# Kernel tuning notes

Hardware: AMD Instinct MI355X
Metric: run time of the kernel (lower is better)

Reference implementation:

```python
import jax, jax.numpy as jnp
import numpy as np

B, LH, LU, H = 32, 1024, 128, 256
NEG = -1e30


def setup_inputs() -> dict:
    key = jax.random.key(0)
    k1, k2, k3, k4, k5, k6 = jax.random.split(key, 6)
    h = jax.random.normal(k1, (B, LH, H), jnp.float32)
    u = jax.random.normal(k2, (B, LU, H), jnp.float32)
    # valid-prefix padding masks (at least half the sequence valid)
    h_len = jax.random.randint(k3, (B,), LH // 2, LH + 1)
    u_len = jax.random.randint(k4, (B,), LU // 2, LU + 1)
    h_mask = jnp.arange(LH)[None, :] < h_len[:, None]
    u_mask = jnp.arange(LU)[None, :] < u_len[:, None]
    # sim_proj: Linear(3H, 1) -> weight flattened to [3H], scalar bias
    w = jax.random.normal(k5, (3 * H,), jnp.float32) / np.sqrt(3 * H)
    b = jax.random.normal(k6, (), jnp.float32)
    return {"h": h, "u": u, "h_mask": h_mask, "u_mask": u_mask, "w": w, "b": b}


def reference(h, u, h_mask, u_mask, w, b):
    d = h.shape[-1]
    w_h, w_u, w_hu = w[:d], w[d:2 * d], w[2 * d:]
    # S[b,i,j] = [h_i; u_j; h_i*u_j] @ w + b  (decomposed, no [B,Lh,Lu,3H] blow-up)
    S = ((h @ w_h)[:, :, None]
         + (u @ w_u)[:, None, :]
         + jnp.einsum('bih,bjh->bij', h * w_hu, u)
         + b)  # [B, Lh, Lu]
    neg = jnp.asarray(NEG, S.dtype)
    # context-to-query attention: softmax over u (dim 2), masked by u_mask
    a_t = jax.nn.softmax(jnp.where(u_mask[:, None, :], S, neg), axis=2)  # [B,Lh,Lu]
    U_tilde = jnp.einsum('bij,bjh->bih', a_t, u)  # [B,Lh,H]
    # query-to-context attention: softmax over h (dim 1), masked by h_mask
    b_t = jax.nn.softmax(jnp.where(h_mask[:, :, None], S, neg), axis=1)  # [B,Lh,Lu]
    b2 = jnp.einsum('biu,bju->bij', b_t, a_t)  # [B,Lh,Lh] = b_t @ a_t^T
    H_tilde = jnp.einsum('bij,bjh->bih', b2, h)  # [B,Lh,H]
    return jnp.concatenate([h, U_tilde, h * U_tilde, h * H_tilde], axis=-1)
```

## Files before the change

### kernel.cpp

```cpp
#include <hip/hip_runtime.h>
#include <hip/hip_bf16.h>

#define BB  32
#define LHH 1024
#define LUU 128
#define HDD 256
#define NEGF (-1e30f)

typedef __attribute__((ext_vector_type(8))) short short8;
typedef __attribute__((ext_vector_type(4))) float f32x4;

static constexpr size_t S_OFF    = 0;
static constexpr size_t UWB_OFF  = S_OFF + (size_t)BB*LHH*LUU;
static constexpr size_t RM_OFF   = UWB_OFF + (size_t)BB*LUU;
static constexpr size_t RI_OFF   = RM_OFF + (size_t)BB*LHH;
static constexpr size_t PM_OFF   = RI_OFF + (size_t)BB*LHH;
static constexpr size_t PS_OFF   = PM_OFF + (size_t)BB*16*LUU;
static constexpr size_t CM_OFF   = PS_OFF + (size_t)BB*16*LUU;
static constexpr size_t CI_OFF   = CM_OFF + (size_t)BB*LUU;
static constexpr size_t UBT_OFF  = CI_OFF + (size_t)BB*LUU;
static constexpr size_t CBT_OFF  = UBT_OFF + (size_t)BB*HDD*LUU/2;
static constexpr size_t FLAG_OFF = CBT_OFF + (size_t)BB*HDD*LUU/2;
static constexpr size_t WS_FLOATS= FLAG_OFF + 1;

__device__ __forceinline__ float mval(const void* p, int idx, int flag) {
    if (flag) return ((const unsigned char*)p)[idx] ? 1.0f : 0.0f;
    return (((const int*)p)[idx] != 0) ? 1.0f : 0.0f;
}
__device__ __forceinline__ float cexpf(float x) { return __expf(fminf(x, 60.0f)); }
__device__ __forceinline__ float grcp(float x)  { return 1.0f / fmaxf(x, 1e-38f); }
__device__ __forceinline__ int swz(int r) { return (r ^ (r >> 2)) & 3; }

__global__ __launch_bounds__(256) void k_uwb(const float* __restrict__ u,
                                             const float* __restrict__ w,
                                             const float* __restrict__ bias,
                                             const unsigned char* __restrict__ hm,
                                             float* __restrict__ ws) {
    if (blockIdx.x == 0 && threadIdx.x == 0)
        reinterpret_cast<int*>(ws)[FLAG_OFF] = (hm[1] != 0) ? 1 : 0;
    int wave = threadIdx.x >> 6;
    int lane = threadIdx.x & 63;
    int idx  = blockIdx.x * 4 + wave;
    int b = idx >> 7, j = idx & 127;
    const float4* u4  = reinterpret_cast<const float4*>(u + ((size_t)(b * LUU + j)) * HDD);
    const float4* wu4 = reinterpret_cast<const float4*>(w + HDD);
    float4 a = u4[lane], c = wu4[lane];
    float s = a.x * c.x + a.y * c.y + a.z * c.z + a.w * c.w;
    #pragma unroll
    for (int off = 32; off; off >>= 1) s += __shfl_xor(s, off);
    if (lane == 0) ws[UWB_OFF + idx] = s + bias[0];
}

__global__ __launch_bounds__(256) void k_uT(const float* __restrict__ u,
                                            float* __restrict__ ws) {
    __shared__ float ls[32][132];
    int b = blockIdx.x, hd0 = blockIdx.y * 32;
    int t = threadIdx.x;
    int hc = t & 7, jj = t >> 3;
    #pragma unroll
    for (int pass = 0; pass < 4; ++pass) {
        int j = jj + pass * 32;
        float4 v = *reinterpret_cast<const float4*>(u + ((size_t)(b * LUU + j)) * HDD + hd0 + hc * 4);
        ls[hc * 4 + 0][j] = v.x; ls[hc * 4 + 1][j] = v.y;
        ls[hc * 4 + 2][j] = v.z; ls[hc * 4 + 3][j] = v.w;
    }
    __syncthreads();
    int r = t >> 3, ck = t & 7;
    short* ubt = reinterpret_cast<short*>(ws + UBT_OFF);
    union { short8 s8; __hip_bfloat16 bh[8]; } pk;
    #pragma unroll
    for (int hhalf = 0; hhalf < 2; ++hhalf) {
        #pragma unroll
        for (int c = 0; c < 8; ++c)
            pk.bh[c] = __float2bfloat16(ls[r][ck * 16 + hhalf * 8 + c]);
        *reinterpret_cast<short8*>(&ubt[((size_t)(b * 256 + hd0 + r)) * 128 + ck * 16 + hhalf * 8]) = pk.s8;
    }
}

__global__ __launch_bounds__(256) void k_Smfma(const float* __restrict__ h,
                                               const float* __restrict__ u,
                                               const void* __restrict__ u_mask,
                                               const void* __restrict__ h_mask,
                                               const float* __restrict__ w,
                                               float* __restrict__ ws) {
    __shared__ __align__(16) short lh[64 * 32];
    __shared__ __align__(16) short lv[128 * 32];
    __shared__ float uwb_l[128], um_l[128], hm_l[64];
    __shared__ float credm[4][128], creds[4][128];

    int b  = blockIdx.x;
    int i0 = blockIdx.y * 64;
    int t  = threadIdx.x;
    int flag = reinterpret_cast<const int*>(ws)[FLAG_OFF];
    int wave = t >> 6, lane = t & 63;
    int lj = lane & 15, lq = lane >> 4;

    if (t < 128) {
        uwb_l[t] = ws[UWB_OFF + b * LUU + t];
        um_l[t]  = mval(u_mask, b * LUU + t, flag);
    } else if (t < 192) {
        hm_l[t - 128] = mval(h_mask, b * LHH + i0 + (t - 128), flag);
    }

    int hrow = t >> 2,  hc = t & 3,  hlc = hc ^ swz(hrow);
    int vrow0 = t >> 2, vc0 = t & 3, vlc0 = vc0 ^ swz(vrow0);
    int vrow1 = (t + 256) >> 2, vc1 = t & 3, vlc1 = vc1 ^ swz(vrow1);
    const float* hsrc = h + ((size_t)(b * LHH + i0 + hrow)) * HDD + hlc * 8;
    const float* us0  = u + ((size_t)(b * LUU + vrow0)) * HDD + vlc0 * 8;
    const float* us1  = u + ((size_t)(b * LUU + vrow1)) * HDD + vlc1 * 8;

    int arow = wave * 16 + lj;
    int a_idx = arow * 32 + ((lq ^ swz(arow)) * 8);
    int b_idx[8];
    #pragma unroll
    for (int n = 0; n < 8; ++n) {
        int j = n * 16 + lj;
        b_idx[n] = j * 32 + ((lq ^ swz(j)) * 8);
    }

    f32x4 acc[8];
    #pragma unroll
    for (int n = 0; n < 8; ++n) acc[n] = (f32x4){0.f, 0.f, 0.f, 0.f};

    for (int step = 0; step < 8; ++step) {
        int k0 = step * 32;
        if (step) __syncthreads();
        {
            float4 f0 = *reinterpret_cast<const float4*>(hsrc + k0);
            float4 f1 = *reinterpret_cast<const float4*>(hsrc + k0 + 4);
            union { short8 s8; __hip_bfloat16 bh[8]; } pk;
            pk.bh[0]=__float2bfloat16(f0.x); pk.bh[1]=__float2bfloat16(f0.y);
            pk.bh[2]=__float2bfloat16(f0.z); pk.bh[3]=__float2bfloat16(f0.w);
            pk.bh[4]=__float2bfloat16(f1.x); pk.bh[5]=__float2bfloat16(f1.y);
            pk.bh[6]=__float2bfloat16(f1.z); pk.bh[7]=__float2bfloat16(f1.w);
            *reinterpret_cast<short8*>(&lh[hrow * 32 + hc * 8]) = pk.s8;
        }
        #pragma unroll
        for (int p = 0; p < 2; ++p) {
            const float* usrc = p ? us1 : us0;
            int vlc = p ? vlc1 : vlc0;
            int vrow = p ? vrow1 : vrow0;
            int vc = p ? vc1 : vc0;
            float4 uu0 = *reinterpret_cast<const float4*>(usrc + k0);
            float4 uu1 = *reinterpret_cast<const float4*>(usrc + k0 + 4);
            float4 wh0 = *reinterpret_cast<const float4*>(w + k0 + vlc * 8);
            float4 wh1 = *reinterpret_cast<const float4*>(w + k0 + vlc * 8 + 4);
            float4 wu0 = *reinterpret_cast<const float4*>(w + 2 * HDD + k0 + vlc * 8);
            float4 wu1 = *reinterpret_cast<const float4*>(w + 2 * HDD + k0 + vlc * 8 + 4);
            union { short8 s8; __hip_bfloat16 bh[8]; } pk;
            pk.bh[0]=__float2bfloat16(wh0.x + wu0.x * uu0.x);
            pk.bh[1]=__float2bfloat16(wh0.y + wu0.y * uu0.y);
            pk.bh[2]=__float2bfloat16(wh0.z + wu0.z * uu0.z);
            pk.bh[3]=__float2bfloat16(wh0.w + wu0.w * uu0.w);
            pk.bh[4]=__float2bfloat16(wh1.x + wu1.x * uu1.x);
            pk.bh[5]=__float2bfloat16(wh1.y + wu1.y * uu1.y);
            pk.bh[6]=__float2bfloat16(wh1.z + wu1.z * uu1.z);
            pk.bh[7]=__float2bfloat16(wh1.w + wu1.w * uu1.w);
            *reinterpret_cast<short8*>(&lv[vrow * 32 + vc * 8]) = pk.s8;
        }
        __syncthreads();
        short8 af = *reinterpret_cast<const short8*>(&lh[a_idx]);
        #pragma unroll
        for (int n = 0; n < 8; ++n) {
            short8 bf = *reinterpret_cast<const short8*>(&lv[b_idx[n]]);
            acc[n] = __builtin_amdgcn_mfma_f32_16x16x32_bf16(af, bf, acc[n], 0, 0, 0);
        }
    }

    float sv[8][4];
    #pragma unroll
    for (int n = 0; n < 8; ++n) {
        float uw = uwb_l[n * 16 + lj];
        #pragma unroll
        for (int q = 0; q < 4; ++q) sv[n][q] = acc[n][q] + uw;
    }
    float umv[8];
    #pragma unroll
    for (int n = 0; n < 8; ++n) umv[n] = um_l[n * 16 + lj];

    #pragma unroll
    for (int q = 0; q < 4; ++q) {
        float ms = NEGF;
        #pragma unroll
        for (int n = 0; n < 8; ++n) ms = fmaxf(ms, umv[n] > 0.f ? sv[n][q] : NEGF);
        #pragma unroll
        for (int off = 8; off; off >>= 1) ms = fmaxf(ms, __shfl_xor(ms, off));
        float e = 0.f;
        #pragma unroll
        for (int n = 0; n < 8; ++n) e += umv[n] * cexpf(sv[n][q] - ms);
        #pragma unroll
        for (int off = 8; off; off >>= 1) e += __shfl_xor(e, off);
        int i = i0 + wave * 16 + lq * 4 + q;
        float* Srow = ws + S_OFF + ((size_t)(b * LHH + i)) * LUU;
        #pragma unroll
        for (int n = 0; n < 8; ++n) Srow[n * 16 + lj] = sv[n][q];
        if (lj == 0) {
            ws[RM_OFF + b * LHH + i] = ms;
            ws[RI_OFF + b * LHH + i] = grcp(e);
        }
    }

    float hmq[4];
    #pragma unroll
    for (int q = 0; q < 4; ++q) hmq[q] = hm_l[wave * 16 + lq * 4 + q];
    #pragma unroll
    for (int n = 0; n < 8; ++n) {
        float cmx = NEGF, csx = 0.f;
        #pragma unroll
        for (int q = 0; q < 4; ++q) {
            if (hmq[q] > 0.f) {
                float x  = sv[n][q];
                float mn = fmaxf(cmx, x);
                csx = csx * cexpf(cmx - mn) + cexpf(x - mn);
                cmx = mn;
            }
        }
        #pragma unroll
        for (int off = 16; off <= 32; off <<= 1) {
            float om = __shfl_xor(cmx, off);
            float os = __shfl_xor(csx, off);
            float mn = fmaxf(cmx, om);
            csx = csx * cexpf(cmx - mn) + os * cexpf(om - mn);
            cmx = mn;
        }
        if (lq == 0) { credm[wave][n * 16 + lj] = cmx; creds[wave][n * 16 + lj] = csx; }
    }
    __syncthreads();
    if (t < 128) {
        float m = credm[0][t], s = creds[0][t];
        #pragma unroll
        for (int wv = 1; wv < 4; ++wv) {
            float om = credm[wv][t], os = creds[wv][t];
            float mn = fmaxf(m, om);
            s = s * cexpf(m - mn) + os * cexpf(om - mn);
            m = mn;
        }
        ws[PM_OFF + (b * 16 + blockIdx.y) * LUU + t] = m;
        ws[PS_OFF + (b * 16 + blockIdx.y) * LUU + t] = s;
    }
}

__global__ __launch_bounds__(256) void k_Cmfma(const float* __restrict__ h,
                                               const void* __restrict__ u_mask,
                                               float* __restrict__ ws) {
    __shared__ __align__(16) short lha[128 * 32];
    __shared__ __align__(16) short lsa[64 * 32];
    int b = blockIdx.x, hd0 = blockIdx.y * 128, u0 = blockIdx.z * 64;
    int t = threadIdx.x;
    int flag = reinterpret_cast<const int*>(ws)[FLAG_OFF];

    if (blockIdx.y == 0 && blockIdx.z == 0 && t < 128) {
        int j = t;
        float m = NEGF;
        #pragma unroll
        for (int c = 0; c < 16; ++c) m = fmaxf(m, ws[PM_OFF + (b * 16 + c) * LUU + j]);
        float s = 0.f;
        #pragma unroll
        for (int c = 0; c < 16; ++c)
            s += ws[PS_OFF + (b * 16 + c) * LUU + j] * cexpf(ws[PM_OFF + (b * 16 + c) * LUU + j] - m);
        ws[CM_OFF + b * LUU + j] = m;
        ws[CI_OFF + b * LUU + j] = grcp(s);
    }

    int wave = t >> 6, lane = t & 63, lj = lane & 15, lq = lane >> 4;
    int hd_r = t & 127, ah = t >> 7;
    int u_r = t & 63, bc = t >> 6;
    float umr = mval(u_mask, b * LUU + u0 + u_r, flag);
    const float* hbp = h + (size_t)b * LHH * HDD + hd0 + hd_r;
    const float* Sbp = ws + S_OFF + (size_t)b * LHH * LUU + u0 + u_r;
    const float* rm = ws + RM_OFF + b * LHH;
    const float* ri = ws + RI_OFF + b * LHH;

    int a_idx[2], b_idx[4];
    #pragma unroll
    for (int m = 0; m < 2; ++m) {
        int row = wave * 32 + m * 16 + lj;
        a_idx[m] = row * 32 + ((lq ^ swz(row)) * 8);
    }
    #pragma unroll
    for (int n = 0; n < 4; ++n) {
        int row = n * 16 + lj;
        b_idx[n] = row * 32 + ((lq ^ swz(row)) * 8);
    }

    f32x4 acc[2][4];
    #pragma unroll
    for (int m = 0; m < 2; ++m)
        #pragma unroll
        for (int n = 0; n < 4; ++n) acc[m][n] = (f32x4){0.f, 0.f, 0.f, 0.f};

    for (int step = 0; step < 32; ++step) {
        int i0 = step * 32;
        if (step) __syncthreads();
        #pragma unroll
        for (int cc = 0; cc < 2; ++cc) {
            int c = ah * 2 + cc, p = c ^ swz(hd_r);
            union { short8 s8; __hip_bfloat16 bh[8]; } pk;
            #pragma unroll
            for (int e = 0; e < 8; ++e)
                pk.bh[e] = __float2bfloat16(hbp[(size_t)(i0 + c * 8 + e) * HDD]);
            *reinterpret_cast<short8*>(&lha[hd_r * 32 + p * 8]) = pk.s8;
        }
        {
            int c = bc, p = c ^ swz(u_r);
            union { short8 s8; __hip_bfloat16 bh[8]; } pk;
            #pragma unroll
            for (int e = 0; e < 8; ++e) {
                int i = i0 + c * 8 + e;
                float sva = Sbp[(size_t)i * LUU];
                pk.bh[e] = __float2bfloat16(umr * cexpf(sva - rm[i]) * ri[i]);
            }
            *reinterpret_cast<short8*>(&lsa[u_r * 32 + p * 8]) = pk.s8;
        }
        __syncthreads();
        short8 af0 = *reinterpret_cast<const short8*>(&lha[a_idx[0]]);
        short8 af1 = *reinterpret_cast<const short8*>(&lha[a_idx[1]]);
        #pragma unroll
        for (int n = 0; n < 4; ++n) {
            short8 bf = *reinterpret_cast<const short8*>(&lsa[b_idx[n]]);
            acc[0][n] = __builtin_amdgcn_mfma_f32_16x16x32_bf16(af0, bf, acc[0][n], 0, 0, 0);
            acc[1][n] = __builtin_amdgcn_mfma_f32_16x16x32_bf16(af1, bf, acc[1][n], 0, 0, 0);
        }
    }

    __hip_bfloat16* cbt = reinterpret_cast<__hip_bfloat16*>(ws + CBT_OFF);
    #pragma unroll
    for (int m = 0; m < 2; ++m)
        #pragma unroll
        for (int q = 0; q < 4; ++q) {
            int hd = hd0 + wave * 32 + m * 16 + lq * 4 + q;
            #pragma unroll
            for (int n = 0; n < 4; ++n) {
                int uu = u0 + n * 16 + lj;
                cbt[(size_t)(b * 256 + hd) * 128 + uu] = __float2bfloat16(acc[m][n][q]);
            }
        }
}

__global__ __launch_bounds__(256) void k_outm(const float* __restrict__ h,
                                              const void* __restrict__ h_mask,
                                              const void* __restrict__ u_mask,
                                              const float* __restrict__ ws,
                                              float* __restrict__ out) {
    __shared__ __align__(16) short la[64 * 32], lb[64 * 32];
    __shared__ __align__(16) short lu[128 * 32], lc[128 * 32];
    __shared__ float rm_l[64], ri_l[64], hm_l[64];
    __shared__ float cm_l[128], ci_l[128], um_l[128];

    int b = blockIdx.x, i0 = blockIdx.y * 64, hd0 = blockIdx.z * 128;
    int t = threadIdx.x;
    int flag = reinterpret_cast<const int*>(ws)[FLAG_OFF];
    int wave = t >> 6, lane = t & 63, lj = lane & 15, lq = lane >> 4;

    if (t < 64) {
        rm_l[t] = ws[RM_OFF + b * LHH + i0 + t];
        ri_l[t] = ws[RI_OFF + b * LHH + i0 + t];
        hm_l[t] = mval(h_mask, b * LHH + i0 + t, flag);
    } else if (t < 192) {
        int j = t - 64;
        cm_l[j] = ws[CM_OFF + b * LUU + j];
        ci_l[j] = ws[CI_OFF + b * LUU + j];
        um_l[j] = mval(u_mask, b * LUU + j, flag);
    }

    const short* ubt = reinterpret_cast<const short*>(ws + UBT_OFF) + ((size_t)(b * 256 + hd0)) * 128;
    const short* cbt = reinterpret_cast<const short*>(ws + CBT_OFF) + ((size_t)(b * 256 + hd0)) * 128;

    int air = t >> 2, ap = t & 3;
    int brow = t >> 1;
    int a_idx = (wave * 16 + lj) * 32 + ((lq ^ swz(wave * 16 + lj)) * 8);
    int b_idx[8];
    #pragma unroll
    for (int n = 0; n < 8; ++n) {
        int r = n * 16 + lj;
        b_idx[n] = r * 32 + ((lq ^ swz(r)) * 8);
    }

    f32x4 aU[8], aH[8];
    #pragma unroll
    for (int n = 0; n < 8; ++n) { aU[n] = (f32x4){0,0,0,0}; aH[n] = (f32x4){0,0,0,0}; }

    for (int step = 0; step < 4; ++step) {
        int j0 = step * 32;
        __syncthreads();
        {
            int lgc = ap ^ swz(air);
            const float* Sp = ws + S_OFF + ((size_t)(b * LHH + i0 + air)) * LUU + j0 + lgc * 8;
            float4 s0 = *reinterpret_cast<const float4*>(Sp);
            float4 s1 = *reinterpret_cast<const float4*>(Sp + 4);
            float rmv = rm_l[air], riv = ri_l[air], hmv = hm_l[air];
            float sv[8] = {s0.x, s0.y, s0.z, s0.w, s1.x, s1.y, s1.z, s1.w};
            union { short8 s8; __hip_bfloat16 bh[8]; } pa, pb;
            #pragma unroll
            for (int c = 0; c < 8; ++c) {
                int j = j0 + lgc * 8 + c;
                pa.bh[c] = __float2bfloat16(um_l[j] * cexpf(sv[c] - rmv) * riv);
                pb.bh[c] = __float2bfloat16(hmv * cexpf(sv[c] - cm_l[j]) * ci_l[j]);
            }
            *reinterpret_cast<short8*>(&la[air * 32 + ap * 8]) = pa.s8;
            *reinterpret_cast<short8*>(&lb[air * 32 + ap * 8]) = pb.s8;
        }
        #pragma unroll
        for (int pp = 0; pp < 2; ++pp) {
            int p = (t & 1) * 2 + pp;
            int lgc = p ^ swz(brow);
            *reinterpret_cast<short8*>(&lu[brow * 32 + p * 8]) =
                *reinterpret_cast<const short8*>(ubt + (size_t)brow * 128 + j0 + lgc * 8);
            *reinterpret_cast<short8*>(&lc[brow * 32 + p * 8]) =
                *reinterpret_cast<const short8*>(cbt + (size_t)brow * 128 + j0 + lgc * 8);
        }
        __syncthreads();
        short8 fa = *reinterpret_cast<const short8*>(&la[a_idx]);
        short8 fb = *reinterpret_cast<const short8*>(&lb[a_idx]);
        #pragma unroll
        for (int n = 0; n < 8; ++n) {
            short8 gu = *reinterpret_cast<const short8*>(&lu[b_idx[n]]);
            short8 gc = *reinterpret_cast<const short8*>(&lc[b_idx[n]]);
            aU[n] = __builtin_amdgcn_mfma_f32_16x16x32_bf16(fa, gu, aU[n], 0, 0, 0);
            aH[n] = __builtin_amdgcn_mfma_f32_16x16x32_bf16(fb, gc, aH[n], 0, 0, 0);
        }
    }

    #pragma unroll
    for (int n = 0; n < 8; ++n) {
        int hd = hd0 + n * 16 + lj;
        #pragma unroll
        for (int q = 0; q < 4; ++q) {
            int i = i0 + wave * 16 + lq * 4 + q;
            float hv = h[((size_t)(b * LHH + i)) * HDD + hd];
            size_t base = ((size_t)(b * LHH + i)) * (4 * HDD) + hd;
            float Uv = aU[n][q], Hv = aH[n][q];
            out[base]           = hv;
            out[base + HDD]     = Uv;
            out[base + 2 * HDD] = hv * Uv;
            out[base + 3 * HDD] = hv * Hv;
        }
    }
}

extern "C" void kernel_launch(void* const* d_in, const int* in_sizes, int n_in,
                              void* d_out, int out_size, void* d_ws, size_t ws_size,
                              hipStream_t stream) {
    const float* h = (const float*)d_in[0];
    const float* u = (const float*)d_in[1];
    const void*  h_mask = d_in[2];
    const void*  u_mask = d_in[3];
    const float* w    = (const float*)d_in[4];
    const float* bias = (const float*)d_in[5];
    float* ws  = (float*)d_ws;
    float* out = (float*)d_out;

    if (ws_size < WS_FLOATS * sizeof(float)) return;

    k_uwb<<<dim3(BB * LUU / 4), 256, 0, stream>>>(u, w, bias, (const unsigned char*)h_mask, ws);
    k_uT<<<dim3(BB, HDD / 32), 256, 0, stream>>>(u, ws);
    k_Smfma<<<dim3(BB, LHH / 64), 256, 0, stream>>>(h, u, u_mask, h_mask, w, ws);
    k_Cmfma<<<dim3(BB, 2, 2), 256, 0, stream>>>(h, u_mask, ws);
    k_outm<<<dim3(BB, LHH / 64, 2), 256, 0, stream>>>(h, h_mask, u_mask, ws, out);
}
```

Before: 95.74 us.

## Store bf16 exp(S-rowmax) instead of fp32 S and precompute u-side bf16 operand

k_Smfma now writes the unnormalised row-softmax numerators exp(S-rowmax) as bf16 instead of raw fp32 S. This halves the intermediate traffic and lets the downstream kernels rebuild both softmaxes by multiplying with per-row and per-column factors (exp(rm), exp(-cm)) instead of recomputing exponentials. The combined w_h + w_hu*u operand is computed once in a prep kernel as bf16 rather than in every S tile block, and the u-mask is applied when C is written. The risk is precision: exp(rm-cm) factors can overflow or underflow, and bf16 rounding of the numerators adds error.

Result: faster. 87.35 us (-8.8%).

```diff
diff --git a/kernel.cpp b/kernel.cpp
--- a/kernel.cpp
+++ b/kernel.cpp
@@ -8,10 +8,11 @@
 #define NEGF (-1e30f)
 
 typedef __attribute__((ext_vector_type(8))) short short8;
+typedef __attribute__((ext_vector_type(4))) short short4v;
 typedef __attribute__((ext_vector_type(4))) float f32x4;
 
-static constexpr size_t S_OFF    = 0;
-static constexpr size_t UWB_OFF  = S_OFF + (size_t)BB*LHH*LUU;
+static constexpr size_t P_OFF    = 0;
+static constexpr size_t UWB_OFF  = P_OFF + (size_t)BB*LHH*LUU/2;
 static constexpr size_t RM_OFF   = UWB_OFF + (size_t)BB*LUU;
 static constexpr size_t RI_OFF   = RM_OFF + (size_t)BB*LHH;
 static constexpr size_t PM_OFF   = RI_OFF + (size_t)BB*LHH;
@@ -20,7 +21,8 @@
 static constexpr size_t CI_OFF   = CM_OFF + (size_t)BB*LUU;
 static constexpr size_t UBT_OFF  = CI_OFF + (size_t)BB*LUU;
 static constexpr size_t CBT_OFF  = UBT_OFF + (size_t)BB*HDD*LUU/2;
-static constexpr size_t FLAG_OFF = CBT_OFF + (size_t)BB*HDD*LUU/2;
+static constexpr size_t VBF_OFF  = CBT_OFF + (size_t)BB*HDD*LUU/2;
+static constexpr size_t FLAG_OFF = VBF_OFF + (size_t)BB*LUU*HDD/2;
 static constexpr size_t WS_FLOATS= FLAG_OFF + 1;
 
 __device__ __forceinline__ float mval(const void* p, int idx, int flag) {
@@ -30,25 +32,40 @@
 __device__ __forceinline__ float cexpf(float x) { return __expf(fminf(x, 60.0f)); }
 __device__ __forceinline__ float grcp(float x)  { return 1.0f / fmaxf(x, 1e-38f); }
 __device__ __forceinline__ int swz(int r) { return (r ^ (r >> 2)) & 3; }
-
-__global__ __launch_bounds__(256) void k_uwb(const float* __restrict__ u,
-                                             const float* __restrict__ w,
-                                             const float* __restrict__ bias,
-                                             const unsigned char* __restrict__ hm,
-                                             float* __restrict__ ws) {
+__device__ __forceinline__ float b2f(short v) {
+    return __uint_as_float(((unsigned)(unsigned short)v) << 16);
+}
+__device__ __forceinline__ short f2b(float x) {
+    __hip_bfloat16 h = __float2bfloat16(x);
+    return *reinterpret_cast<short*>(&h);
+}
+
+__global__ __launch_bounds__(256) void k_prep(const float* __restrict__ u,
+                                              const float* __restrict__ w,
+                                              const float* __restrict__ bias,
+                                              const unsigned char* __restrict__ hm,
+                                              float* __restrict__ ws) {
     if (blockIdx.x == 0 && threadIdx.x == 0)
         reinterpret_cast<int*>(ws)[FLAG_OFF] = (hm[1] != 0) ? 1 : 0;
     int wave = threadIdx.x >> 6;
     int lane = threadIdx.x & 63;
     int idx  = blockIdx.x * 4 + wave;
     int b = idx >> 7, j = idx & 127;
-    const float4* u4  = reinterpret_cast<const float4*>(u + ((size_t)(b * LUU + j)) * HDD);
-    const float4* wu4 = reinterpret_cast<const float4*>(w + HDD);
-    float4 a = u4[lane], c = wu4[lane];
-    float s = a.x * c.x + a.y * c.y + a.z * c.z + a.w * c.w;
+    float4 uu   = reinterpret_cast<const float4*>(u + ((size_t)(b * LUU + j)) * HDD)[lane];
+    float4 whv  = reinterpret_cast<const float4*>(w)[lane];
+    float4 wuv  = reinterpret_cast<const float4*>(w + HDD)[lane];
+    float4 whuv = reinterpret_cast<const float4*>(w + 2 * HDD)[lane];
+    float s = uu.x * wuv.x + uu.y * wuv.y + uu.z * wuv.z + uu.w * wuv.w;
     #pragma unroll
     for (int off = 32; off; off >>= 1) s += __shfl_xor(s, off);
     if (lane == 0) ws[UWB_OFF + idx] = s + bias[0];
+    union { short4v s4; __hip_bfloat16 bh[4]; } pk;
+    pk.bh[0] = __float2bfloat16(whv.x + whuv.x * uu.x);
+    pk.bh[1] = __float2bfloat16(whv.y + whuv.y * uu.y);
+    pk.bh[2] = __float2bfloat16(whv.z + whuv.z * uu.z);
+    pk.bh[3] = __float2bfloat16(whv.w + whuv.w * uu.w);
+    short* vbf = reinterpret_cast<short*>(ws + VBF_OFF);
+    *reinterpret_cast<short4v*>(&vbf[((size_t)(b * LUU + j)) * HDD + lane * 4]) = pk.s4;
 }
 
 __global__ __launch_bounds__(256) void k_uT(const float* __restrict__ u,
@@ -78,10 +95,8 @@
 }
 
 __global__ __launch_bounds__(256) void k_Smfma(const float* __restrict__ h,
-                                               const float* __restrict__ u,
                                                const void* __restrict__ u_mask,
                                                const void* __restrict__ h_mask,
-                                               const float* __restrict__ w,
                                                float* __restrict__ ws) {
     __shared__ __align__(16) short lh[64 * 32];
     __shared__ __align__(16) short lv[128 * 32];
@@ -106,8 +121,9 @@
     int vrow0 = t >> 2, vc0 = t & 3, vlc0 = vc0 ^ swz(vrow0);
     int vrow1 = (t + 256) >> 2, vc1 = t & 3, vlc1 = vc1 ^ swz(vrow1);
     const float* hsrc = h + ((size_t)(b * LHH + i0 + hrow)) * HDD + hlc * 8;
-    const float* us0  = u + ((size_t)(b * LUU + vrow0)) * HDD + vlc0 * 8;
-    const float* us1  = u + ((size_t)(b * LUU + vrow1)) * HDD + vlc1 * 8;
+    const short* vbf  = reinterpret_cast<const short*>(ws + VBF_OFF);
+    const short* vsrc0 = vbf + ((size_t)(b * LUU + vrow0)) * HDD + vlc0 * 8;
+    const short* vsrc1 = vbf + ((size_t)(b * LUU + vrow1)) * HDD + vlc1 * 8;
 
     int arow = wave * 16 + lj;
     int a_idx = arow * 32 + ((lq ^ swz(arow)) * 8);
@@ -135,29 +151,10 @@
             pk.bh[6]=__float2bfloat16(f1.z); pk.bh[7]=__float2bfloat16(f1.w);
             *reinterpret_cast<short8*>(&lh[hrow * 32 + hc * 8]) = pk.s8;
         }
-        #pragma unroll
-        for (int p = 0; p < 2; ++p) {
-            const float* usrc = p ? us1 : us0;
-            int vlc = p ? vlc1 : vlc0;
-            int vrow = p ? vrow1 : vrow0;
-            int vc = p ? vc1 : vc0;
-            float4 uu0 = *reinterpret_cast<const float4*>(usrc + k0);
-            float4 uu1 = *reinterpret_cast<const float4*>(usrc + k0 + 4);
-            float4 wh0 = *reinterpret_cast<const float4*>(w + k0 + vlc * 8);
-            float4 wh1 = *reinterpret_cast<const float4*>(w + k0 + vlc * 8 + 4);
-            float4 wu0 = *reinterpret_cast<const float4*>(w + 2 * HDD + k0 + vlc * 8);
-            float4 wu1 = *reinterpret_cast<const float4*>(w + 2 * HDD + k0 + vlc * 8 + 4);
-            union { short8 s8; __hip_bfloat16 bh[8]; } pk;
-            pk.bh[0]=__float2bfloat16(wh0.x + wu0.x * uu0.x);
-            pk.bh[1]=__float2bfloat16(wh0.y + wu0.y * uu0.y);
-            pk.bh[2]=__float2bfloat16(wh0.z + wu0.z * uu0.z);
-            pk.bh[3]=__float2bfloat16(wh0.w + wu0.w * uu0.w);
-            pk.bh[4]=__float2bfloat16(wh1.x + wu1.x * uu1.x);
-            pk.bh[5]=__float2bfloat16(wh1.y + wu1.y * uu1.y);
-            pk.bh[6]=__float2bfloat16(wh1.z + wu1.z * uu1.z);
-            pk.bh[7]=__float2bfloat16(wh1.w + wu1.w * uu1.w);
-            *reinterpret_cast<short8*>(&lv[vrow * 32 + vc * 8]) = pk.s8;
-        }
+        *reinterpret_cast<short8*>(&lv[vrow0 * 32 + vc0 * 8]) =
+            *reinterpret_cast<const short8*>(vsrc0 + k0);
+        *reinterpret_cast<short8*>(&lv[vrow1 * 32 + vc1 * 8]) =
+            *reinterpret_cast<const short8*>(vsrc1 + k0);
         __syncthreads();
         short8 af = *reinterpret_cast<const short8*>(&lh[a_idx]);
         #pragma unroll
@@ -178,6 +175,7 @@
     #pragma unroll
     for (int n = 0; n < 8; ++n) umv[n] = um_l[n * 16 + lj];
 
+    short* Pg = reinterpret_cast<short*>(ws + P_OFF);
     #pragma unroll
     for (int q = 0; q < 4; ++q) {
         float ms = NEGF;
@@ -185,15 +183,15 @@
         for (int n = 0; n < 8; ++n) ms = fmaxf(ms, umv[n] > 0.f ? sv[n][q] : NEGF);
         #pragma unroll
         for (int off = 8; off; off >>= 1) ms = fmaxf(ms, __shfl_xor(ms, off));
-        float e = 0.f;
-        #pragma unroll
-        for (int n = 0; n < 8; ++n) e += umv[n] * cexpf(sv[n][q] - ms);
+        float pe[8], e = 0.f;
+        #pragma unroll
+        for (int n = 0; n < 8; ++n) { pe[n] = cexpf(sv[n][q] - ms); e += umv[n] * pe[n]; }
         #pragma unroll
         for (int off = 8; off; off >>= 1) e += __shfl_xor(e, off);
         int i = i0 + wave * 16 + lq * 4 + q;
-        float* Srow = ws + S_OFF + ((size_t)(b * LHH + i)) * LUU;
-        #pragma unroll
-        for (int n = 0; n < 8; ++n) Srow[n * 16 + lj] = sv[n][q];
+        short* Prow = Pg + ((size_t)(b * LHH + i)) * LUU;
+        #pragma unroll
+        for (int n = 0; n < 8; ++n) Prow[n * 16 + lj] = f2b(pe[n]);
         if (lj == 0) {
             ws[RM_OFF + b * LHH + i] = ms;
             ws[RI_OFF + b * LHH + i] = grcp(e);
@@ -245,12 +243,15 @@
                                                float* __restrict__ ws) {
     __shared__ __align__(16) short lha[128 * 32];
     __shared__ __align__(16) short lsa[64 * 32];
+    __shared__ float um_s[64];
     int b = blockIdx.x, hd0 = blockIdx.y * 128, u0 = blockIdx.z * 64;
     int t = threadIdx.x;
     int flag = reinterpret_cast<const int*>(ws)[FLAG_OFF];
 
-    if (blockIdx.y == 0 && blockIdx.z == 0 && t < 128) {
-        int j = t;
+    if (t < 64) um_s[t] = mval(u_mask, b * LUU + u0 + t, flag);
+
+    if (blockIdx.y == 0 && blockIdx.z == 0 && t >= 64 && t < 192) {
+        int j = t - 64;
         float m = NEGF;
         #pragma unroll
         for (int c = 0; c < 16; ++c) m = fmaxf(m, ws[PM_OFF + (b * 16 + c) * LUU + j]);
@@ -265,10 +266,8 @@
     int wave = t >> 6, lane = t & 63, lj = lane & 15, lq = lane >> 4;
     int hd_r = t & 127, ah = t >> 7;
     int u_r = t & 63, bc = t >> 6;
-    float umr = mval(u_mask, b * LUU + u0 + u_r, flag);
     const float* hbp = h + (size_t)b * LHH * HDD + hd0 + hd_r;
-    const float* Sbp = ws + S_OFF + (size_t)b * LHH * LUU + u0 + u_r;
-    const float* rm = ws + RM_OFF + b * LHH;
+    const short* Pbp = reinterpret_cast<const short*>(ws + P_OFF) + (size_t)b * LHH * LUU + u0 + u_r;
     const float* ri = ws + RI_OFF + b * LHH;
 
     int a_idx[2], b_idx[4];
@@ -307,8 +306,8 @@
             #pragma unroll
             for (int e = 0; e < 8; ++e) {
                 int i = i0 + c * 8 + e;
-                float sva = Sbp[(size_t)i * LUU];
-                pk.bh[e] = __float2bfloat16(umr * cexpf(sva - rm[i]) * ri[i]);
+                float pv = b2f(Pbp[(size_t)i * LUU]);
+                pk.bh[e] = __float2bfloat16(pv * ri[i]);
             }
             *reinterpret_cast<short8*>(&lsa[u_r * 32 + p * 8]) = pk.s8;
         }
@@ -331,8 +330,9 @@
             int hd = hd0 + wave * 32 + m * 16 + lq * 4 + q;
             #pragma unroll
             for (int n = 0; n < 4; ++n) {
-                int uu = u0 + n * 16 + lj;
-                cbt[(size_t)(b * 256 + hd) * 128 + uu] = __float2bfloat16(acc[m][n][q]);
+                int uu = n * 16 + lj;
+                cbt[(size_t)(b * 256 + hd) * 128 + u0 + uu] =
+                    __float2bfloat16(acc[m][n][q] * um_s[uu]);
             }
         }
 }
@@ -344,8 +344,8 @@
                                               float* __restrict__ out) {
     __shared__ __align__(16) short la[64 * 32], lb[64 * 32];
     __shared__ __align__(16) short lu[128 * 32], lc[128 * 32];
-    __shared__ float rm_l[64], ri_l[64], hm_l[64];
-    __shared__ float cm_l[128], ci_l[128], um_l[128];
+    __shared__ float ri_l[64], R_l[64];
+    __shared__ float um_l[128], Cc_l[128];
 
     int b = blockIdx.x, i0 = blockIdx.y * 64, hd0 = blockIdx.z * 128;
     int t = threadIdx.x;
@@ -353,16 +353,17 @@
     int wave = t >> 6, lane = t & 63, lj = lane & 15, lq = lane >> 4;
 
     if (t < 64) {
-        rm_l[t] = ws[RM_OFF + b * LHH + i0 + t];
+        float rmv = ws[RM_OFF + b * LHH + i0 + t];
         ri_l[t] = ws[RI_OFF + b * LHH + i0 + t];
-        hm_l[t] = mval(h_mask, b * LHH + i0 + t, flag);
+        R_l[t]  = mval(h_mask, b * LHH + i0 + t, flag) * cexpf(rmv);
     } else if (t < 192) {
         int j = t - 64;
-        cm_l[j] = ws[CM_OFF + b * LUU + j];
-        ci_l[j] = ws[CI_OFF + b * LUU + j];
+        float cmv = ws[CM_OFF + b * LUU + j];
+        Cc_l[j] = cexpf(-cmv) * ws[CI_OFF + b * LUU + j];
         um_l[j] = mval(u_mask, b * LUU + j, flag);
     }
 
+    const short* Pbase = reinterpret_cast<const short*>(ws + P_OFF) + (size_t)b * LHH * LUU;
     const short* ubt = reinterpret_cast<const short*>(ws + UBT_OFF) + ((size_t)(b * 256 + hd0)) * 128;
     const short* cbt = reinterpret_cast<const short*>(ws + CBT_OFF) + ((size_t)(b * 256 + hd0)) * 128;
 
@@ -385,17 +386,16 @@
         __syncthreads();
         {
             int lgc = ap ^ swz(air);
-            const float* Sp = ws + S_OFF + ((size_t)(b * LHH + i0 + air)) * LUU + j0 + lgc * 8;
-            float4 s0 = *reinterpret_cast<const float4*>(Sp);
-            float4 s1 = *reinterpret_cast<const float4*>(Sp + 4);
-            float rmv = rm_l[air], riv = ri_l[air], hmv = hm_l[air];
-            float sv[8] = {s0.x, s0.y, s0.z, s0.w, s1.x, s1.y, s1.z, s1.w};
+            short8 pv8 = *reinterpret_cast<const short8*>(
+                Pbase + (size_t)(i0 + air) * LUU + j0 + lgc * 8);
+            float riv = ri_l[air], Rv = R_l[air];
             union { short8 s8; __hip_bfloat16 bh[8]; } pa, pb;
             #pragma unroll
             for (int c = 0; c < 8; ++c) {
                 int j = j0 + lgc * 8 + c;
-                pa.bh[c] = __float2bfloat16(um_l[j] * cexpf(sv[c] - rmv) * riv);
-                pb.bh[c] = __float2bfloat16(hmv * cexpf(sv[c] - cm_l[j]) * ci_l[j]);
+                float p = b2f(pv8[c]);
+                pa.bh[c] = __float2bfloat16(p * um_l[j] * riv);
+                pb.bh[c] = __float2bfloat16(p * Rv * Cc_l[j]);
             }
             *reinterpret_cast<short8*>(&la[air * 32 + ap * 8]) = pa.s8;
             *reinterpret_cast<short8*>(&lb[air * 32 + ap * 8]) = pb.s8;
@@ -452,9 +452,9 @@
 
     if (ws_size < WS_FLOATS * sizeof(float)) return;
 
-    k_uwb<<<dim3(BB * LUU / 4), 256, 0, stream>>>(u, w, bias, (const unsigned char*)h_mask, ws);
+    k_prep<<<dim3(BB * LUU / 4), 256, 0, stream>>>(u, w, bias, (const unsigned char*)h_mask, ws);
     k_uT<<<dim3(BB, HDD / 32), 256, 0, stream>>>(u, ws);
-    k_Smfma<<<dim3(BB, LHH / 64), 256, 0, stream>>>(h, u, u_mask, h_mask, w, ws);
+    k_Smfma<<<dim3(BB, LHH / 64), 256, 0, stream>>>(h, u_mask, h_mask, ws);
     k_Cmfma<<<dim3(BB, 2, 2), 256, 0, stream>>>(h, u_mask, ws);
     k_outm<<<dim3(BB, LHH / 64, 2), 256, 0, stream>>>(h, h_mask, u_mask, ws, out);
 }
```
